# Optimization experiments

Hardware: AMD Instinct MI355X
Metric: run time of the kernel (lower is better)

The kernel has to match this reference:

```python
import jax, jax.numpy as jnp
import numpy as np

B, IN_DIM, OUT_DIM = 4096, 2048, 2048
EMA_M = 0.95
LN_EPS = 1e-5


def setup_inputs() -> dict:
    key = jax.random.key(0)
    ks = jax.random.split(key, 8)
    x = jax.random.normal(ks[0], (B, IN_DIM), dtype=jnp.float32)
    # W_slow is orthogonal-init in torch (gain 0.5); scaled gaussian is a fine stand-in for math testing
    W_slow = jax.random.normal(ks[1], (OUT_DIM, IN_DIM), dtype=jnp.float32) * (0.5 / np.sqrt(IN_DIM))
    # buffers start at zero in torch; use small nonzero values so the medium/fast GEMMs are exercised
    W_medium = jax.random.normal(ks[2], (OUT_DIM, IN_DIM), dtype=jnp.float32) * 0.01
    W_fast = jax.random.normal(ks[3], (OUT_DIM, IN_DIM), dtype=jnp.float32) * 0.01
    ln_gamma = jnp.ones((OUT_DIM,), jnp.float32) + 0.1 * jax.random.normal(ks[4], (OUT_DIM,), dtype=jnp.float32)
    ln_beta = 0.1 * jax.random.normal(ks[5], (OUT_DIM,), dtype=jnp.float32)
    pc_w1 = jax.random.normal(ks[6], (8, 3), dtype=jnp.float32) * 0.5
    pc_b1 = jnp.zeros((8,), jnp.float32)
    pc_w2 = jax.random.normal(ks[7], (1, 8), dtype=jnp.float32) * 0.5
    pc_b2 = jnp.full((1,), -1.5, jnp.float32)  # torch fills last Linear bias with -1.5
    ema_mean = jnp.zeros((1,), jnp.float32)
    ema_std = jnp.ones((1,), jnp.float32)
    return {"x": x, "W_slow": W_slow, "W_medium": W_medium, "W_fast": W_fast,
            "ln_gamma": ln_gamma, "ln_beta": ln_beta,
            "pc_w1": pc_w1, "pc_b1": pc_b1, "pc_w2": pc_w2, "pc_b2": pc_b2,
            "ema_mean": ema_mean, "ema_std": ema_std}


def reference(x, W_slow, W_medium, W_fast, ln_gamma, ln_beta,
              pc_w1, pc_b1, pc_w2, pc_b2, ema_mean, ema_std):
    xc = jnp.clip(x, -5.0, 5.0)
    slow_out = jnp.clip(xc @ W_slow.T, -10.0, 10.0)
    pre_act = jnp.clip(slow_out + xc @ W_medium.T + xc @ W_fast.T, -10.0, 10.0)  # [B, OUT]

    batch_mean = pre_act.mean(axis=1, keepdims=True)                      # [B,1]
    batch_std = jnp.maximum(pre_act.std(axis=1, keepdims=True), 1e-6)     # [B,1], ddof=0

    # EMA buffer update (no-grad in torch); clamps applied after update
    new_mean = jnp.clip(EMA_M * ema_mean + (1.0 - EMA_M) * batch_mean.mean(), -0.5, 0.5)
    new_std = jnp.clip(EMA_M * ema_std + (1.0 - EMA_M) * batch_std.mean(), 0.1, 1.5)
    homeostasis = new_std / (jnp.abs(new_mean) + 1e-6)                    # [1]

    stats = jnp.concatenate([batch_mean, batch_std,
                             jnp.broadcast_to(homeostasis[None, :], (batch_mean.shape[0], 1))], axis=1)  # [B,3]
    h = jax.nn.gelu(stats @ pc_w1.T + pc_b1, approximate=False)           # torch GELU is exact erf
    learned_plasticity = jax.nn.sigmoid(h @ pc_w2.T + pc_b2)[:, 0]        # [B] (does not affect `out`)
    _ = learned_plasticity  # kept for fidelity with original compute graph

    # LayerNorm over last dim, eps=1e-5
    mu = pre_act.mean(axis=-1, keepdims=True)
    var = pre_act.var(axis=-1, keepdims=True)
    normed = (pre_act - mu) * jax.lax.rsqrt(var + LN_EPS) * ln_gamma + ln_beta
    out = 5.0 * jnp.tanh(normed / 5.0)
    return out
```

## Files before the change

### kernel.cpp

```cpp
#include <hip/hip_runtime.h>
#include <hip/hip_bf16.h>

#define BDIM    4096
#define IN_DIM  2048
#define OUT_DIM 2048

typedef __attribute__((ext_vector_type(4))) float  floatx4;
typedef __attribute__((ext_vector_type(8))) short  bf16x8;

__device__ __forceinline__ unsigned short f2bf(float f) {
    union { float f; unsigned u; } v; v.f = f;
    unsigned r = v.u + 0x7FFFu + ((v.u >> 16) & 1u);
    return (unsigned short)(r >> 16);
}

__device__ __forceinline__ float bf2f(unsigned short h) {
    union { unsigned u; float f; } v; v.u = (unsigned)h << 16;
    return v.f;
}

__device__ __forceinline__ void async16(const unsigned short* g, unsigned short* l) {
    __builtin_amdgcn_global_load_lds(
        (const __attribute__((address_space(1))) unsigned int*)g,
        (__attribute__((address_space(3))) unsigned int*)l,
        16, 0, 0);
}

__global__ __launch_bounds__(256) void prep(const float* __restrict__ x,
                                            const float* __restrict__ Ws,
                                            const float* __restrict__ Wm,
                                            const float* __restrict__ Wf,
                                            unsigned short* __restrict__ xc,
                                            unsigned short* __restrict__ bsum) {
    int b = blockIdx.x;
    if (b < 8192) {
        int i = b * 256 + threadIdx.x;
        float4 v = ((const float4*)x)[i];
        ushort4 o;
        o.x = f2bf(fminf(fmaxf(v.x, -5.f), 5.f));
        o.y = f2bf(fminf(fmaxf(v.y, -5.f), 5.f));
        o.z = f2bf(fminf(fmaxf(v.z, -5.f), 5.f));
        o.w = f2bf(fminf(fmaxf(v.w, -5.f), 5.f));
        ((ushort4*)xc)[i] = o;
    } else {
        int i = (b - 8192) * 256 + threadIdx.x;
        float4 s = ((const float4*)Ws)[i];
        float4 m = ((const float4*)Wm)[i];
        float4 f = ((const float4*)Wf)[i];
        ushort4 o;
        o.x = f2bf(s.x + m.x + f.x);
        o.y = f2bf(s.y + m.y + f.y);
        o.z = f2bf(s.z + m.z + f.z);
        o.w = f2bf(s.w + m.w + f.w);
        ((ushort4*)bsum)[i] = o;
    }
}

#define TILE  128
#define BK    64
#define ITERS (IN_DIM / BK)

#define MEMBAR() asm volatile("" ::: "memory")

__global__ __launch_bounds__(256, 2) void gemm_bt(const unsigned short* __restrict__ A,
                                                  const unsigned short* __restrict__ B,
                                                  unsigned short* __restrict__ C) {
    constexpr int N = OUT_DIM, K = IN_DIM;
    __shared__ __align__(16) unsigned short As[2 * TILE * BK];
    __shared__ __align__(16) unsigned short Bs[2 * TILE * BK];

    const int tid  = threadIdx.x;
    const int lane = tid & 63;
    const int wave = tid >> 6;
    const int wm   = (wave >> 1) * 64;
    const int wn   = (wave & 1) * 64;
    const int rowBlock = blockIdx.y * TILE;
    const int colBlock = blockIdx.x * TILE;

    const int sRow = tid >> 3;
    const int sSeg = (tid & 7) ^ (sRow & 7);
    const unsigned short* aSrc = A + (size_t)(rowBlock + sRow) * K + sSeg * 8;
    const unsigned short* bSrc = B + (size_t)(colBlock + sRow) * K + sSeg * 8;

    floatx4 acc[4][4] = {};

    const int fragRow = lane & 15;
    const int quad    = lane >> 4;
    const int l7      = lane & 7;

    auto stage = [&](int t, int p) {
        unsigned short* ad = As + p * TILE * BK + tid * 8;
        unsigned short* bd = Bs + p * TILE * BK + tid * 8;
        const unsigned short* ag = aSrc + t * BK;
        const unsigned short* bg = bSrc + t * BK;
#pragma unroll
        for (int r = 0; r < 4; r++)
            async16(ag + (size_t)(r * 32) * K, ad + r * 32 * BK);
#pragma unroll
        for (int r = 0; r < 4; r++)
            async16(bg + (size_t)(r * 32) * K, bd + r * 32 * BK);
    };

    stage(0, 0);
    stage(1, 1);
    __builtin_amdgcn_s_waitcnt(0xF78);
    MEMBAR();
    __builtin_amdgcn_s_barrier();
    MEMBAR();

    for (int k = 0; k < ITERS; k++) {
        const int p = k & 1;
        const unsigned short* Ab = As + p * TILE * BK;
        const unsigned short* Bb = Bs + p * TILE * BK;

#pragma unroll
        for (int kk = 0; kk < 2; kk++) {
            const int xs = ((quad + kk * 4) ^ l7) << 3;
            bf16x8 af[4], bfr[4];
#pragma unroll
            for (int i = 0; i < 4; i++) {
                af[i]  = *(const bf16x8*)(Ab + (wm + i * 16 + fragRow) * BK + xs);
                bfr[i] = *(const bf16x8*)(Bb + (wn + i * 16 + fragRow) * BK + xs);
            }
#pragma unroll
            for (int i = 0; i < 4; i++)
#pragma unroll
                for (int j = 0; j < 4; j++)
                    acc[i][j] = __builtin_amdgcn_mfma_f32_16x16x32_bf16(af[i], bfr[j], acc[i][j], 0, 0, 0);
        }

        MEMBAR();
        __builtin_amdgcn_s_barrier();
        MEMBAR();
        if (k < ITERS - 2) {
            stage(k + 2, p);
            __builtin_amdgcn_s_waitcnt(0xF78);
        } else {
            __builtin_amdgcn_s_waitcnt(0xF70);
        }
        MEMBAR();
        __builtin_amdgcn_s_barrier();
        MEMBAR();
    }

    const int cCol = colBlock + wn + (lane & 15);
    const int cRow = rowBlock + wm + (lane >> 4) * 4;
#pragma unroll
    for (int i = 0; i < 4; i++) {
#pragma unroll
        for (int j = 0; j < 4; j++) {
            const int col = cCol + j * 16;
            const int rb  = cRow + i * 16;
#pragma unroll
            for (int r = 0; r < 4; r++)
                C[(size_t)(rb + r) * N + col] = f2bf(acc[i][j][r]);
        }
    }
}

__global__ __launch_bounds__(256) void ln_kernel(const unsigned short* __restrict__ C,
                                                 const float* __restrict__ gamma,
                                                 const float* __restrict__ beta,
                                                 float* __restrict__ out) {
    const int row = blockIdx.x;
    const int tid = threadIdx.x;
    __shared__ float wsum[4], wsq[4];

    const uint2* Cr = (const uint2*)(C + (size_t)row * OUT_DIM);

    float4 p[2];
    float sum = 0.f, sq = 0.f;
#pragma unroll
    for (int it = 0; it < 2; it++) {
        uint2 u = Cr[tid + it * 256];
        float4 q;
        q.x = bf2f((unsigned short)(u.x & 0xFFFF));
        q.y = bf2f((unsigned short)(u.x >> 16));
        q.z = bf2f((unsigned short)(u.y & 0xFFFF));
        q.w = bf2f((unsigned short)(u.y >> 16));
        q.x = fminf(fmaxf(q.x, -10.f), 10.f);
        q.y = fminf(fmaxf(q.y, -10.f), 10.f);
        q.z = fminf(fmaxf(q.z, -10.f), 10.f);
        q.w = fminf(fmaxf(q.w, -10.f), 10.f);
        p[it] = q;
        sum += q.x + q.y + q.z + q.w;
        sq  += q.x * q.x + q.y * q.y + q.z * q.z + q.w * q.w;
    }
#pragma unroll
    for (int off = 32; off > 0; off >>= 1) {
        sum += __shfl_down(sum, off);
        sq  += __shfl_down(sq,  off);
    }
    if ((tid & 63) == 0) { wsum[tid >> 6] = sum; wsq[tid >> 6] = sq; }
    __syncthreads();
    const float tsum = wsum[0] + wsum[1] + wsum[2] + wsum[3];
    const float tsq  = wsq[0]  + wsq[1]  + wsq[2]  + wsq[3];
    const float mu   = tsum * (1.0f / OUT_DIM);
    const float var  = tsq * (1.0f / OUT_DIM) - mu * mu;
    const float inv  = rsqrtf(var + 1e-5f);

#pragma unroll
    for (int it = 0; it < 2; it++) {
        int i = tid + it * 256;
        float4 q = p[it];
        float4 g = *(const float4*)(gamma + i * 4);
        float4 b = *(const float4*)(beta + i * 4);
        float4 o;
        float zx = (q.x - mu) * inv * g.x + b.x;
        float zy = (q.y - mu) * inv * g.y + b.y;
        float zz = (q.z - mu) * inv * g.z + b.z;
        float zw = (q.w - mu) * inv * g.w + b.w;
        o.x = 5.f * (1.f - 2.f / (__expf(0.4f * zx) + 1.f));
        o.y = 5.f * (1.f - 2.f / (__expf(0.4f * zy) + 1.f));
        o.z = 5.f * (1.f - 2.f / (__expf(0.4f * zz) + 1.f));
        o.w = 5.f * (1.f - 2.f / (__expf(0.4f * zw) + 1.f));
        *(float4*)(out + (size_t)row * OUT_DIM + i * 4) = o;
    }
}

extern "C" void kernel_launch(void* const* d_in, const int* in_sizes, int n_in,
                              void* d_out, int out_size, void* d_ws, size_t ws_size,
                              hipStream_t stream) {
    const float* x     = (const float*)d_in[0];
    const float* Ws    = (const float*)d_in[1];
    const float* Wm    = (const float*)d_in[2];
    const float* Wf    = (const float*)d_in[3];
    const float* gamma = (const float*)d_in[4];
    const float* beta  = (const float*)d_in[5];
    float* out = (float*)d_out;

    char* ws = (char*)d_ws;
    unsigned short* xc   = (unsigned short*)ws;
    unsigned short* bsum = (unsigned short*)(ws + (size_t)16 * 1024 * 1024);
    unsigned short* Cbuf = (unsigned short*)(ws + (size_t)24 * 1024 * 1024);

    prep<<<12288, 256, 0, stream>>>(x, Ws, Wm, Wf, xc, bsum);
    dim3 g(OUT_DIM / TILE, BDIM / TILE);
    gemm_bt<<<g, 256, 0, stream>>>(xc, bsum, Cbuf);
    ln_kernel<<<BDIM, 256, 0, stream>>>(Cbuf, gamma, beta, out);
}
```

Measured before the change: 181.7 us.

## Enlarge GEMM block tile to 256x128 with BK=32 and new LDS swizzle

Changes the GEMM block tile from 128x128 to 256x128 and halves the K step to 32. Each wave now computes a 128x64 sub-tile with 32 accumulators. The LDS swizzle and async staging pattern are reworked for 64-byte rows, and the grid is reduced to 16x16 blocks. This aims to raise arithmetic intensity per LDS load and cut global traffic per FLOP. In exchange it doubles the barrier count, raises register pressure, and leaves only 256 blocks with one block per CU, which may underfill 256 CUs and give poor latency hiding.

```diff
diff --git a/kernel.cpp b/kernel.cpp
--- a/kernel.cpp
+++ b/kernel.cpp
@@ -56,85 +56,83 @@
     }
 }
 
-#define TILE  128
-#define BK    64
-#define ITERS (IN_DIM / BK)
+#define TILE_M 256
+#define TILE_N 128
+#define BK     32
+#define ITERS  (IN_DIM / BK)
 
 #define MEMBAR() asm volatile("" ::: "memory")
 
-__global__ __launch_bounds__(256, 2) void gemm_bt(const unsigned short* __restrict__ A,
+__global__ __launch_bounds__(256, 1) void gemm_bt(const unsigned short* __restrict__ A,
                                                   const unsigned short* __restrict__ B,
                                                   unsigned short* __restrict__ C) {
     constexpr int N = OUT_DIM, K = IN_DIM;
-    __shared__ __align__(16) unsigned short As[2 * TILE * BK];
-    __shared__ __align__(16) unsigned short Bs[2 * TILE * BK];
+    __shared__ __align__(16) unsigned short As[2 * TILE_M * BK];
+    __shared__ __align__(16) unsigned short Bs[2 * TILE_N * BK];
 
     const int tid  = threadIdx.x;
     const int lane = tid & 63;
     const int wave = tid >> 6;
-    const int wm   = (wave >> 1) * 64;
+    const int wm   = (wave >> 1) * 128;
     const int wn   = (wave & 1) * 64;
-    const int rowBlock = blockIdx.y * TILE;
-    const int colBlock = blockIdx.x * TILE;
-
-    const int sRow = tid >> 3;
-    const int sSeg = (tid & 7) ^ (sRow & 7);
+    const int rowBlock = blockIdx.y * TILE_M;
+    const int colBlock = blockIdx.x * TILE_N;
+
+    const int sRow = tid >> 2;
+    const int sSeg = (tid & 3) ^ ((sRow ^ (sRow >> 2)) & 3);
     const unsigned short* aSrc = A + (size_t)(rowBlock + sRow) * K + sSeg * 8;
     const unsigned short* bSrc = B + (size_t)(colBlock + sRow) * K + sSeg * 8;
 
-    floatx4 acc[4][4] = {};
+    floatx4 acc[8][4] = {};
 
     const int fragRow = lane & 15;
     const int quad    = lane >> 4;
-    const int l7      = lane & 7;
+    const int xs      = ((quad ^ ((fragRow ^ (fragRow >> 2)) & 3))) << 3;
 
     auto stage = [&](int t, int p) {
-        unsigned short* ad = As + p * TILE * BK + tid * 8;
-        unsigned short* bd = Bs + p * TILE * BK + tid * 8;
+        unsigned short* ad = As + p * TILE_M * BK + tid * 8;
+        unsigned short* bd = Bs + p * TILE_N * BK + tid * 8;
         const unsigned short* ag = aSrc + t * BK;
         const unsigned short* bg = bSrc + t * BK;
 #pragma unroll
         for (int r = 0; r < 4; r++)
-            async16(ag + (size_t)(r * 32) * K, ad + r * 32 * BK);
-#pragma unroll
-        for (int r = 0; r < 4; r++)
-            async16(bg + (size_t)(r * 32) * K, bd + r * 32 * BK);
+            async16(ag + (size_t)(r * 64) * K, ad + r * 64 * BK);
+#pragma unroll
+        for (int r = 0; r < 2; r++)
+            async16(bg + (size_t)(r * 64) * K, bd + r * 64 * BK);
     };
 
     stage(0, 0);
     stage(1, 1);
-    __builtin_amdgcn_s_waitcnt(0xF78);
+    __builtin_amdgcn_s_waitcnt(0xF76);
     MEMBAR();
     __builtin_amdgcn_s_barrier();
     MEMBAR();
 
     for (int k = 0; k < ITERS; k++) {
-        const int p = k & 1;
-        const unsigned short* Ab = As + p * TILE * BK;
-        const unsigned short* Bb = Bs + p * TILE * BK;
-
-#pragma unroll
-        for (int kk = 0; kk < 2; kk++) {
-            const int xs = ((quad + kk * 4) ^ l7) << 3;
-            bf16x8 af[4], bfr[4];
-#pragma unroll
-            for (int i = 0; i < 4; i++) {
-                af[i]  = *(const bf16x8*)(Ab + (wm + i * 16 + fragRow) * BK + xs);
-                bfr[i] = *(const bf16x8*)(Bb + (wn + i * 16 + fragRow) * BK + xs);
-            }
-#pragma unroll
-            for (int i = 0; i < 4; i++)
-#pragma unroll
-                for (int j = 0; j < 4; j++)
-                    acc[i][j] = __builtin_amdgcn_mfma_f32_16x16x32_bf16(af[i], bfr[j], acc[i][j], 0, 0, 0);
-        }
-
+        const unsigned short* Ab = As + (k & 1) * TILE_M * BK;
+        const unsigned short* Bb = Bs + (k & 1) * TILE_N * BK;
+
+        bf16x8 af[8], bfr[4];
+#pragma unroll
+        for (int i = 0; i < 8; i++)
+            af[i] = *(const bf16x8*)(Ab + (wm + i * 16 + fragRow) * BK + xs);
+#pragma unroll
+        for (int j = 0; j < 4; j++)
+            bfr[j] = *(const bf16x8*)(Bb + (wn + j * 16 + fragRow) * BK + xs);
+#pragma unroll
+        for (int i = 0; i < 8; i++)
+#pragma unroll
+            for (int j = 0; j < 4; j++)
+                acc[i][j] = __builtin_amdgcn_mfma_f32_16x16x32_bf16(af[i], bfr[j], acc[i][j], 0, 0, 0);
+
+        if (k == ITERS - 1) break;
         MEMBAR();
         __builtin_amdgcn_s_barrier();
         MEMBAR();
-        if (k < ITERS - 2) {
-            stage(k + 2, p);
-            __builtin_amdgcn_s_waitcnt(0xF78);
+        if (k + 2 < ITERS) {
+            stage(k + 2, k & 1);
+            __builtin_amdgcn_s_waitcnt(0xF76);
         } else {
             __builtin_amdgcn_s_waitcnt(0xF70);
         }
@@ -144,9 +142,9 @@
     }
 
     const int cCol = colBlock + wn + (lane & 15);
-    const int cRow = rowBlock + wm + (lane >> 4) * 4;
-#pragma unroll
-    for (int i = 0; i < 4; i++) {
+    const int cRow = rowBlock + wm + quad * 4;
+#pragma unroll
+    for (int i = 0; i < 8; i++) {
 #pragma unroll
         for (int j = 0; j < 4; j++) {
             const int col = cCol + j * 16;
@@ -235,7 +233,7 @@
     unsigned short* Cbuf = (unsigned short*)(ws + (size_t)24 * 1024 * 1024);
 
     prep<<<12288, 256, 0, stream>>>(x, Ws, Wm, Wf, xc, bsum);
-    dim3 g(OUT_DIM / TILE, BDIM / TILE);
+    dim3 g(OUT_DIM / TILE_N, BDIM / TILE_M);
     gemm_bt<<<g, 256, 0, stream>>>(xc, bsum, Cbuf);
     ln_kernel<<<BDIM, 256, 0, stream>>>(Cbuf, gamma, beta, out);
 }
```

After: 217.2 us. 19.6% more time.

## Split GEMM K dimension in two, single-buffer B tile, sum partials in LayerNorm

Applied to the files above, without the earlier changes.

The GEMM grid gains a z dimension that splits K into two halves. Each half writes its own bf16 partial C buffer, and the LayerNorm kernel sums the two partials before clamping. The B tile is now single-buffered to cut LDS use, so occupancy can rise to 3 blocks per CU. The aim is more blocks in flight and better latency hiding, at the cost of twice the C write and read traffic, extra bf16 rounding on the partials, and B loads that are less overlapped with compute.

```diff
diff --git a/kernel.cpp b/kernel.cpp
--- a/kernel.cpp
+++ b/kernel.cpp
@@ -56,18 +56,20 @@
     }
 }
 
-#define TILE  128
-#define BK    64
-#define ITERS (IN_DIM / BK)
+#define TILE   128
+#define BK     64
+#define KSPLIT 2
+#define KHALF  (IN_DIM / KSPLIT)
+#define ITERS  (KHALF / BK)
 
 #define MEMBAR() asm volatile("" ::: "memory")
 
-__global__ __launch_bounds__(256, 2) void gemm_bt(const unsigned short* __restrict__ A,
+__global__ __launch_bounds__(256, 3) void gemm_bt(const unsigned short* __restrict__ A,
                                                   const unsigned short* __restrict__ B,
-                                                  unsigned short* __restrict__ C) {
+                                                  unsigned short* __restrict__ Cpart) {
     constexpr int N = OUT_DIM, K = IN_DIM;
     __shared__ __align__(16) unsigned short As[2 * TILE * BK];
-    __shared__ __align__(16) unsigned short Bs[2 * TILE * BK];
+    __shared__ __align__(16) unsigned short Bs[TILE * BK];
 
     const int tid  = threadIdx.x;
     const int lane = tid & 63;
@@ -76,11 +78,13 @@
     const int wn   = (wave & 1) * 64;
     const int rowBlock = blockIdx.y * TILE;
     const int colBlock = blockIdx.x * TILE;
+    const int kBase    = blockIdx.z * KHALF;
+    unsigned short* C = Cpart + (size_t)blockIdx.z * BDIM * OUT_DIM;
 
     const int sRow = tid >> 3;
     const int sSeg = (tid & 7) ^ (sRow & 7);
-    const unsigned short* aSrc = A + (size_t)(rowBlock + sRow) * K + sSeg * 8;
-    const unsigned short* bSrc = B + (size_t)(colBlock + sRow) * K + sSeg * 8;
+    const unsigned short* aSrc = A + (size_t)(rowBlock + sRow) * K + kBase + sSeg * 8;
+    const unsigned short* bSrc = B + (size_t)(colBlock + sRow) * K + kBase + sSeg * 8;
 
     floatx4 acc[4][4] = {};
 
@@ -88,30 +92,31 @@
     const int quad    = lane >> 4;
     const int l7      = lane & 7;
 
-    auto stage = [&](int t, int p) {
+    auto stageA = [&](int t, int p) {
         unsigned short* ad = As + p * TILE * BK + tid * 8;
-        unsigned short* bd = Bs + p * TILE * BK + tid * 8;
         const unsigned short* ag = aSrc + t * BK;
-        const unsigned short* bg = bSrc + t * BK;
 #pragma unroll
         for (int r = 0; r < 4; r++)
             async16(ag + (size_t)(r * 32) * K, ad + r * 32 * BK);
+    };
+    auto stageB = [&](int t) {
+        unsigned short* bd = Bs + tid * 8;
+        const unsigned short* bg = bSrc + t * BK;
 #pragma unroll
         for (int r = 0; r < 4; r++)
             async16(bg + (size_t)(r * 32) * K, bd + r * 32 * BK);
     };
 
-    stage(0, 0);
-    stage(1, 1);
-    __builtin_amdgcn_s_waitcnt(0xF78);
+    stageB(0);
+    stageA(0, 0);
+    stageA(1, 1);
+    __builtin_amdgcn_s_waitcnt(0xF74);
     MEMBAR();
     __builtin_amdgcn_s_barrier();
     MEMBAR();
 
     for (int k = 0; k < ITERS; k++) {
-        const int p = k & 1;
-        const unsigned short* Ab = As + p * TILE * BK;
-        const unsigned short* Bb = Bs + p * TILE * BK;
+        const unsigned short* Ab = As + (k & 1) * TILE * BK;
 
 #pragma unroll
         for (int kk = 0; kk < 2; kk++) {
@@ -120,7 +125,7 @@
 #pragma unroll
             for (int i = 0; i < 4; i++) {
                 af[i]  = *(const bf16x8*)(Ab + (wm + i * 16 + fragRow) * BK + xs);
-                bfr[i] = *(const bf16x8*)(Bb + (wn + i * 16 + fragRow) * BK + xs);
+                bfr[i] = *(const bf16x8*)(Bs + (wn + i * 16 + fragRow) * BK + xs);
             }
 #pragma unroll
             for (int i = 0; i < 4; i++)
@@ -129,12 +134,14 @@
                     acc[i][j] = __builtin_amdgcn_mfma_f32_16x16x32_bf16(af[i], bfr[j], acc[i][j], 0, 0, 0);
         }
 
+        if (k == ITERS - 1) break;
         MEMBAR();
         __builtin_amdgcn_s_barrier();
         MEMBAR();
-        if (k < ITERS - 2) {
-            stage(k + 2, p);
-            __builtin_amdgcn_s_waitcnt(0xF78);
+        stageB(k + 1);
+        if (k + 2 < ITERS) {
+            stageA(k + 2, k & 1);
+            __builtin_amdgcn_s_waitcnt(0xF74);
         } else {
             __builtin_amdgcn_s_waitcnt(0xF70);
         }
@@ -144,7 +151,7 @@
     }
 
     const int cCol = colBlock + wn + (lane & 15);
-    const int cRow = rowBlock + wm + (lane >> 4) * 4;
+    const int cRow = rowBlock + wm + quad * 4;
 #pragma unroll
     for (int i = 0; i < 4; i++) {
 #pragma unroll
@@ -158,7 +165,7 @@
     }
 }
 
-__global__ __launch_bounds__(256) void ln_kernel(const unsigned short* __restrict__ C,
+__global__ __launch_bounds__(256) void ln_kernel(const unsigned short* __restrict__ Cpart,
                                                  const float* __restrict__ gamma,
                                                  const float* __restrict__ beta,
                                                  float* __restrict__ out) {
@@ -166,18 +173,20 @@
     const int tid = threadIdx.x;
     __shared__ float wsum[4], wsq[4];
 
-    const uint2* Cr = (const uint2*)(C + (size_t)row * OUT_DIM);
+    const uint2* Ca = (const uint2*)(Cpart + (size_t)row * OUT_DIM);
+    const uint2* Cb = (const uint2*)(Cpart + (size_t)BDIM * OUT_DIM + (size_t)row * OUT_DIM);
 
     float4 p[2];
     float sum = 0.f, sq = 0.f;
 #pragma unroll
     for (int it = 0; it < 2; it++) {
-        uint2 u = Cr[tid + it * 256];
+        uint2 ua = Ca[tid + it * 256];
+        uint2 ub = Cb[tid + it * 256];
         float4 q;
-        q.x = bf2f((unsigned short)(u.x & 0xFFFF));
-        q.y = bf2f((unsigned short)(u.x >> 16));
-        q.z = bf2f((unsigned short)(u.y & 0xFFFF));
-        q.w = bf2f((unsigned short)(u.y >> 16));
+        q.x = bf2f((unsigned short)(ua.x & 0xFFFF)) + bf2f((unsigned short)(ub.x & 0xFFFF));
+        q.y = bf2f((unsigned short)(ua.x >> 16))    + bf2f((unsigned short)(ub.x >> 16));
+        q.z = bf2f((unsigned short)(ua.y & 0xFFFF)) + bf2f((unsigned short)(ub.y & 0xFFFF));
+        q.w = bf2f((unsigned short)(ua.y >> 16))    + bf2f((unsigned short)(ub.y >> 16));
         q.x = fminf(fmaxf(q.x, -10.f), 10.f);
         q.y = fminf(fmaxf(q.y, -10.f), 10.f);
         q.z = fminf(fmaxf(q.z, -10.f), 10.f);
@@ -235,7 +244,7 @@
     unsigned short* Cbuf = (unsigned short*)(ws + (size_t)24 * 1024 * 1024);
 
     prep<<<12288, 256, 0, stream>>>(x, Ws, Wm, Wf, xc, bsum);
-    dim3 g(OUT_DIM / TILE, BDIM / TILE);
+    dim3 g(OUT_DIM / TILE, BDIM / TILE, KSPLIT);
     gemm_bt<<<g, 256, 0, stream>>>(xc, bsum, Cbuf);
     ln_kernel<<<BDIM, 256, 0, stream>>>(Cbuf, gamma, beta, out);
 }
```

Measured after the change: 185.3 us. 1.02x slower.
